# Kernel optimization log

Hardware: AMD Instinct MI355X
Metric: run time of the kernel (lower is better)

## Reference

```python
import jax, jax.numpy as jnp
import numpy as np

VAR = 1.0
STD = float(np.sqrt(VAR))


def setup_inputs() -> dict:
    key = jax.random.key(0)
    k1, k2 = jax.random.split(key)
    n, c = 262144, 100
    scores = jax.random.normal(k1, (n, c), dtype=jnp.float32)
    labels = jax.random.randint(k2, (n,), 0, c, dtype=jnp.int64)
    return {"scores": scores, "labels": labels}


def reference(scores, labels):
    n, c = scores.shape
    # Gaussian pdf over class indices, centered at each label (re_encode_label)
    x = jnp.arange(c, dtype=scores.dtype)[None, :]            # (1, c)
    mu = labels.astype(scores.dtype)[:, None]                  # (n, 1)
    inv_norm = 1.0 / (STD * np.sqrt(2.0 * np.pi))
    code = inv_norm * jnp.exp(-0.5 * ((x - mu) / STD) ** 2)    # (n, c)
    # target distribution: softmax over the (unnormalized) pdf values
    target = jax.nn.softmax(code, axis=1)
    logsfmx = jax.nn.log_softmax(scores, axis=1)
    # KLDivLoss(reduction='batchmean'): sum(target * (log target - input)) / n
    kl = jnp.sum(target * (jnp.log(target) - logsfmx)) / n
    return kl
```

## Files before the change

### kernel.cpp

```cpp
#include <hip/hip_runtime.h>
#include <math.h>

#define C 100
#define RPP 16
#define WAVES 4
#define PASSES 4
#define ROWS_PER_BLOCK_PASS (WAVES * RPP)
#define INV_NORM 0.3989422804014327f
#define DMAX 6

#define QSWZ(x, pat) __int_as_float(__builtin_amdgcn_ds_swizzle(__float_as_int(x), (pat)))

__global__ __launch_bounds__(256, 6) void kl_main(
    const float* __restrict__ scores,
    const int*   __restrict__ labels,
    float* __restrict__ out, int n, float inv_n)
{
    __shared__ float sl[WAVES][RPP * C];
    __shared__ float wpart[WAVES];

    const int tid  = threadIdx.x;
    const int wave = tid >> 6;
    const int lane = tid & 63;
    const int r    = lane >> 2;
    const int sub  = lane & 3;

    const float wfar = __expf(-INV_NORM);
    float wp[DMAX + 1], wcp[DMAX + 1];
    #pragma unroll
    for (int k = 0; k <= DMAX; ++k) {
        float code = INV_NORM * __expf(-0.5f * (float)(k * k));
        float w    = __expf(code - INV_NORM);
        wp[k]  = w - wfar;
        wcp[k] = w * code;
    }

    float* mys = sl[wave];
    float acc = 0.f;

    for (int pass = 0; pass < PASSES; ++pass) {
        const int rowBase = (blockIdx.x * PASSES + pass) * ROWS_PER_BLOCK_PASS
                          + wave * RPP;
        const int remRows = min(RPP, max(0, n - rowBase));
        const int nf4     = remRows * (C / 4);

        const float4* gsrc = (const float4*)(scores + (size_t)rowBase * C);
        float4 v[7];
        #pragma unroll
        for (int c = 0; c < 7; ++c) {
            int g = lane + 64 * c;
            v[c] = (g < nf4) ? gsrc[g] : make_float4(0.f, 0.f, 0.f, 0.f);
        }
        const int myrow = rowBase + r;
        const int mu    = (myrow < n) ? labels[myrow] : 0;

        float4* st = (float4*)mys;
        #pragma unroll
        for (int c = 0; c < 7; ++c) {
            int g = lane + 64 * c;
            if (g < RPP * (C / 4)) st[g] = v[c];
        }

        const float* sp = &mys[r * C];

        float se = 0.f, rs = 0.f;
        const float* spl = sp + sub * 25;
        #pragma unroll
        for (int i = 0; i < 25; ++i) {
            float s = spl[i];
            se += __expf(s);
            rs += s;
        }
        se += QSWZ(se, 0x80B1); rs += QSWZ(rs, 0x80B1);
        se += QSWZ(se, 0x804E); rs += QSWZ(rs, 0x804E);

        float dotw = 0.f, csum = (float)C * wfar, dotc = 0.f;
        #pragma unroll
        for (int d = -DMAX; d <= DMAX; ++d) {
            int idx   = mu + d;
            bool ok   = (unsigned)idx < (unsigned)C;
            float s   = sp[min(max(idx, 0), C - 1)];
            int   a   = (d < 0) ? -d : d;
            float wv  = ok ? wp[a]  : 0.f;
            float wcv = ok ? wcp[a] : 0.f;
            dotw = fmaf(wv, s, dotw);
            csum += wv;
            dotc += wcv;
        }

        if (sub == 0 && myrow < n) {
            float rc  = 1.0f / csum;
            float dot = fmaf(wfar, rs, dotw);
            acc += (dotc - dot) * rc - INV_NORM - __logf(csum) + __logf(se);
        }
    }

    #pragma unroll
    for (int off = 32; off > 0; off >>= 1)
        acc += __shfl_xor(acc, off, 64);
    if (lane == 0) wpart[wave] = acc;
    __syncthreads();
    if (tid == 0)
        atomicAdd(out, (wpart[0] + wpart[1] + wpart[2] + wpart[3]) * inv_n);
}

extern "C" void kernel_launch(void* const* d_in, const int* in_sizes, int n_in,
                              void* d_out, int out_size, void* d_ws, size_t ws_size,
                              hipStream_t stream)
{
    const float* scores = (const float*)d_in[0];
    const int*   labels = (const int*)d_in[1];
    float*       out    = (float*)d_out;

    int n = in_sizes[0] / C;

    hipMemsetAsync(d_out, 0, sizeof(float) * (size_t)out_size, stream);

    int rows_per_block = PASSES * ROWS_PER_BLOCK_PASS;
    int blocks = (n + rows_per_block - 1) / rows_per_block;
    kl_main<<<blocks, 256, 0, stream>>>(scores, labels, out, n, 1.0f / (float)n);
}
```

Before: 159.1 us.

## Double-buffer global loads across passes and remap rows to contiguous per-wave spans

Software-pipelines the per-wave loop so the next pass's scores and labels are issued into a second register set before the current pass is reduced, hiding global load latency. Each wave now owns a contiguous span of rows instead of interleaving with other waves per pass. Gaussian weight tables become compile-time constants, ds_swizzle quad reductions become DPP adds, and the launch-bounds occupancy hint drops from 6 to 4 blocks to make room for the doubled register buffers. The cost is higher register pressure and possibly lower occupancy.

```diff
diff --git a/kernel.cpp b/kernel.cpp
--- a/kernel.cpp
+++ b/kernel.cpp
@@ -5,13 +5,21 @@
 #define RPP 16
 #define WAVES 4
 #define PASSES 4
-#define ROWS_PER_BLOCK_PASS (WAVES * RPP)
+#define ROWS_PER_WAVE  (RPP * PASSES)
+#define ROWS_PER_BLOCK (WAVES * ROWS_PER_WAVE)
+#define NF4P (RPP * C / 4)
 #define INV_NORM 0.3989422804014327f
-#define DMAX 6
+#define WFAR     0.67102943f
 
-#define QSWZ(x, pat) __int_as_float(__builtin_amdgcn_ds_swizzle(__float_as_int(x), (pat)))
+__device__ __forceinline__ float quad_sum(float x) {
+    x += __int_as_float(__builtin_amdgcn_update_dpp(
+            0, __float_as_int(x), 0xB1, 0xF, 0xF, true));
+    x += __int_as_float(__builtin_amdgcn_update_dpp(
+            0, __float_as_int(x), 0x4E, 0xF, 0xF, true));
+    return x;
+}
 
-__global__ __launch_bounds__(256, 6) void kl_main(
+__global__ __launch_bounds__(256, 4) void kl_main(
     const float* __restrict__ scores,
     const int*   __restrict__ labels,
     float* __restrict__ out, int n, float inv_n)
@@ -20,80 +28,80 @@
     __shared__ float wpart[WAVES];
 
     const int tid  = threadIdx.x;
-    const int wave = tid >> 6;
-    const int lane = tid & 63;
-    const int r    = lane >> 2;
-    const int sub  = lane & 3;
+    const int wave = tid >> 6, lane = tid & 63;
+    const int r    = lane >> 2, sub  = lane & 3;
+    float* const mys = sl[wave];
 
-    const float wfar = __expf(-INV_NORM);
-    float wp[DMAX + 1], wcp[DMAX + 1];
-    #pragma unroll
-    for (int k = 0; k <= DMAX; ++k) {
-        float code = INV_NORM * __expf(-0.5f * (float)(k * k));
-        float w    = __expf(code - INV_NORM);
-        wp[k]  = w - wfar;
-        wcp[k] = w * code;
-    }
+    const int waveRow0 = blockIdx.x * ROWS_PER_BLOCK + wave * ROWS_PER_WAVE;
 
-    float* mys = sl[wave];
+    float4 va[7], vb[7];
+    int mua = 0, mub = 0;
     float acc = 0.f;
 
-    for (int pass = 0; pass < PASSES; ++pass) {
-        const int rowBase = (blockIdx.x * PASSES + pass) * ROWS_PER_BLOCK_PASS
-                          + wave * RPP;
-        const int remRows = min(RPP, max(0, n - rowBase));
-        const int nf4     = remRows * (C / 4);
-
-        const float4* gsrc = (const float4*)(scores + (size_t)rowBase * C);
-        float4 v[7];
+    auto issue = [&](float4* v, int p, int& mu) {
+        const int rowBase = waveRow0 + p * RPP;
+        const int nf4 = min(RPP, max(0, n - rowBase)) * (C / 4);
+        const float4* g = (const float4*)(scores + (size_t)rowBase * C);
         #pragma unroll
         for (int c = 0; c < 7; ++c) {
-            int g = lane + 64 * c;
-            v[c] = (g < nf4) ? gsrc[g] : make_float4(0.f, 0.f, 0.f, 0.f);
+            int i = lane + 64 * c;
+            v[c] = (i < nf4) ? g[i] : make_float4(0.f, 0.f, 0.f, 0.f);
         }
-        const int myrow = rowBase + r;
-        const int mu    = (myrow < n) ? labels[myrow] : 0;
+        int myrow = rowBase + r;
+        mu = (myrow < n) ? labels[myrow] : 0;
+    };
 
+    auto consume = [&](const float4* v, int p, int mu) {
         float4* st = (float4*)mys;
         #pragma unroll
         for (int c = 0; c < 7; ++c) {
-            int g = lane + 64 * c;
-            if (g < RPP * (C / 4)) st[g] = v[c];
+            int i = lane + 64 * c;
+            if (i < NF4P) st[i] = v[c];
         }
-
-        const float* sp = &mys[r * C];
-
+        const float* sp  = &mys[r * C];
+        const float* spl = sp + sub * 25;
         float se = 0.f, rs = 0.f;
-        const float* spl = sp + sub * 25;
         #pragma unroll
         for (int i = 0; i < 25; ++i) {
             float s = spl[i];
             se += __expf(s);
             rs += s;
         }
-        se += QSWZ(se, 0x80B1); rs += QSWZ(rs, 0x80B1);
-        se += QSWZ(se, 0x804E); rs += QSWZ(rs, 0x804E);
+        se = quad_sum(se);
+        rs = quad_sum(rs);
 
-        float dotw = 0.f, csum = (float)C * wfar, dotc = 0.f;
+        const float WP[7] = {0.32897057f, 0.18369895f, 0.03722540f,
+            0.00298049f, 8.9804e-5f, 9.9763e-7f, 4.0768e-9f};
+        const float WC[7] = {0.39894228f, 0.20681926f, 0.03823936f,
+            0.00298711f, 8.9816e-5f, 9.9765e-7f, 4.0768e-9f};
+        float dotw = 0.f, csum = 100.f * WFAR, dotc = 0.f;
         #pragma unroll
-        for (int d = -DMAX; d <= DMAX; ++d) {
-            int idx   = mu + d;
-            bool ok   = (unsigned)idx < (unsigned)C;
-            float s   = sp[min(max(idx, 0), C - 1)];
-            int   a   = (d < 0) ? -d : d;
-            float wv  = ok ? wp[a]  : 0.f;
-            float wcv = ok ? wcp[a] : 0.f;
-            dotw = fmaf(wv, s, dotw);
+        for (int d = -6; d <= 6; ++d) {
+            int idx  = mu + d;
+            bool ok  = (unsigned)idx < (unsigned)C;
+            float s  = sp[min(max(idx, 0), C - 1)];
+            int a    = d < 0 ? -d : d;
+            float wv = ok ? WP[a] : 0.f;
+            dotw  = fmaf(wv, s, dotw);
             csum += wv;
-            dotc += wcv;
+            dotc += ok ? WC[a] : 0.f;
         }
 
+        int myrow = waveRow0 + p * RPP + r;
         if (sub == 0 && myrow < n) {
-            float rc  = 1.0f / csum;
-            float dot = fmaf(wfar, rs, dotw);
-            acc += (dotc - dot) * rc - INV_NORM - __logf(csum) + __logf(se);
+            float dot = fmaf(WFAR, rs, dotw);
+            acc += (dotc - dot) / csum - INV_NORM - __logf(csum) + __logf(se);
         }
-    }
+    };
+
+    issue(va, 0, mua);
+    issue(vb, 1, mub);
+    consume(va, 0, mua);
+    issue(va, 2, mua);
+    consume(vb, 1, mub);
+    issue(vb, 3, mub);
+    consume(va, 2, mua);
+    consume(vb, 3, mub);
 
     #pragma unroll
     for (int off = 32; off > 0; off >>= 1)
@@ -116,7 +124,6 @@
 
     hipMemsetAsync(d_out, 0, sizeof(float) * (size_t)out_size, stream);
 
-    int rows_per_block = PASSES * ROWS_PER_BLOCK_PASS;
-    int blocks = (n + rows_per_block - 1) / rows_per_block;
+    int blocks = (n + ROWS_PER_BLOCK - 1) / ROWS_PER_BLOCK;
     kl_main<<<blocks, 256, 0, stream>>>(scores, labels, out, n, 1.0f / (float)n);
 }
```

Result: faster. 155.9 us (-2.0%).
